# Performance work log

Measured on AMD Instinct MI355X. Metric: run time of the kernel, lower is better.

The kernel has to match this reference:

```python
import jax, jax.numpy as jnp
import numpy as np

B, S, H = 2, 2048, 2048
N_HEADS, N_KV = 16, 4
HEAD_DIM = H // N_HEADS  # 128
ROPE_THETA = 10000.0


def _rope_tables(seq_len, dim, theta):
    inv_freq = 1.0 / (theta ** (jnp.arange(0, dim, 2, dtype=jnp.float32) / dim))
    t = jnp.arange(seq_len, dtype=jnp.float32)
    freqs = jnp.outer(t, inv_freq)                 # [S, dim/2]
    emb = jnp.concatenate([freqs, freqs], axis=-1)  # [S, dim]
    return jnp.cos(emb), jnp.sin(emb)


def _rotate_half(x):
    x1, x2 = jnp.split(x, 2, axis=-1)
    return jnp.concatenate([-x2, x1], axis=-1)


def setup_inputs() -> dict:
    key = jax.random.key(0)
    ks = jax.random.split(key, 8)
    sc = 0.02
    return {
        "hidden_states": jax.random.normal(ks[0], (B, S, H), jnp.float32),
        "Wq": jax.random.normal(ks[1], (H, N_HEADS * HEAD_DIM), jnp.float32) * sc,
        "bq": jax.random.normal(ks[2], (N_HEADS * HEAD_DIM,), jnp.float32) * sc,
        "Wk": jax.random.normal(ks[3], (H, N_KV * HEAD_DIM), jnp.float32) * sc,
        "bk": jax.random.normal(ks[4], (N_KV * HEAD_DIM,), jnp.float32) * sc,
        "Wv": jax.random.normal(ks[5], (H, N_KV * HEAD_DIM), jnp.float32) * sc,
        "bv": jax.random.normal(ks[6], (N_KV * HEAD_DIM,), jnp.float32) * sc,
        "Wo": jax.random.normal(ks[7], (N_HEADS * HEAD_DIM, H), jnp.float32) * sc,
    }


def reference(hidden_states, Wq, bq, Wk, bk, Wv, bv, Wo):
    bsz, q_len, _ = hidden_states.shape
    q = hidden_states @ Wq + bq  # [B,S,nH*D]
    k = hidden_states @ Wk + bk  # [B,S,nKV*D]
    v = hidden_states @ Wv + bv
    q = q.reshape(bsz, q_len, N_HEADS, HEAD_DIM).transpose(0, 2, 1, 3)   # [B,nH,S,D]
    k = k.reshape(bsz, q_len, N_KV, HEAD_DIM).transpose(0, 2, 1, 3)      # [B,nKV,S,D]
    v = v.reshape(bsz, q_len, N_KV, HEAD_DIM).transpose(0, 2, 1, 3)

    cos, sin = _rope_tables(q_len, HEAD_DIM, ROPE_THETA)  # [S,D]
    cos = cos[None, None].astype(q.dtype)  # [1,1,S,D]
    sin = sin[None, None].astype(q.dtype)
    q = q * cos + _rotate_half(q) * sin
    k = k * cos + _rotate_half(k) * sin

    groups = N_HEADS // N_KV
    k_rep = jnp.repeat(k, groups, axis=1)  # [B,nH,S,D]
    v_rep = jnp.repeat(v, groups, axis=1)

    scale = 1.0 / np.sqrt(HEAD_DIM)
    scores = jnp.einsum("bhqd,bhkd->bhqk", q, k_rep) * scale
    attn = jax.nn.softmax(scores.astype(jnp.float32), axis=-1).astype(q.dtype)
    out = jnp.einsum("bhqk,bhkd->bhqd", attn, v_rep)
    out = out.transpose(0, 2, 1, 3).reshape(bsz, q_len, N_HEADS * HEAD_DIM)
    return out @ Wo
```

## Files before the change

kernel.cpp:

```cpp
#include <hip/hip_runtime.h>
#include <stdint.h>
#include <math.h>

typedef unsigned int u32;
typedef __bf16 bf16x8 __attribute__((ext_vector_type(8)));
typedef float  f32x4  __attribute__((ext_vector_type(4)));
typedef float  f32x16 __attribute__((ext_vector_type(16)));
typedef unsigned int u32x4 __attribute__((ext_vector_type(4)));
typedef unsigned short u16x4 __attribute__((ext_vector_type(4)));
typedef unsigned short u16x8 __attribute__((ext_vector_type(8)));

#define DEV __device__ __forceinline__

DEV unsigned short f2b(float f) {
  u32 x = __builtin_bit_cast(u32, f);
  u32 r = (x + 0x7fffu + ((x >> 16) & 1u)) >> 16;
  return (unsigned short)r;
}
DEV float b2f(unsigned short u) { return __builtin_bit_cast(float, ((u32)u) << 16); }

DEV u32 cvtpk_bf16(float lo, float hi) {
  u32 r;
  asm("v_cvt_pk_bf16_f32 %0, %1, %2" : "=v"(r) : "v"(lo), "v"(hi));
  return r;
}
DEV void pl32swap(u32& a, u32& b) {
  asm("v_permlane32_swap_b32 %0, %1" : "+v"(a), "+v"(b));
}

DEV void gl2lds16(const void* g, void* l) {
  __builtin_amdgcn_global_load_lds((const __attribute__((address_space(1))) u32*)g,
                                   (__attribute__((address_space(3))) u32*)l, 16, 0, 0);
}

__global__ __launch_bounds__(256) void prep_k(
    const float* __restrict__ X, const float* __restrict__ Wq,
    const float* __restrict__ Wk, const float* __restrict__ Wv,
    const float* __restrict__ Wo, float* __restrict__ ct, float* __restrict__ st,
    unsigned short* __restrict__ Xp, unsigned short* __restrict__ Wcat,
    unsigned short* __restrict__ Wop) {
  __shared__ float t[32][33];
  const int tid = threadIdx.x;
  int bx = blockIdx.x;
  if (bx < 512) {
    int i = (bx << 8) + tid;
    int d = i & 63;
    float inv = powf(10000.0f, -(float)d / 64.0f);
    float a = (float)(i >> 6) * inv;
    ct[i] = cosf(a);
    st[i] = sinf(a);
    return;
  }
  bx -= 512;
  if (bx < 4096) {
    int i = (bx << 8) + tid;
    int k8 = i & 255, m = i >> 8;
    const float4* p = (const float4*)(X + (size_t)m * 2048 + (k8 << 3));
    float4 v0 = p[0], v1 = p[1];
    u16x8 r = { f2b(v0.x), f2b(v0.y), f2b(v0.z), f2b(v0.w),
                f2b(v1.x), f2b(v1.y), f2b(v1.z), f2b(v1.w) };
    int kt = k8 >> 2, ko = (k8 & 3) << 3;
    *(u16x8*)(Xp + ((size_t)kt * 4096 + m) * 32 + ko) = r;
    return;
  }
  bx -= 4096;
  int wx = bx % 160, wy = bx / 160;
  const float* src; unsigned short* dst; int Nd, Ncat, ncOff, nb;
  if (wx < 64)       { src = Wq; dst = Wcat; Nd = 2048; Ncat = 3072; ncOff = 0;    nb = wx; }
  else if (wx < 80)  { src = Wk; dst = Wcat; Nd = 512;  Ncat = 3072; ncOff = 2048; nb = wx - 64; }
  else if (wx < 96)  { src = Wv; dst = Wcat; Nd = 512;  Ncat = 3072; ncOff = 2560; nb = wx - 80; }
  else               { src = Wo; dst = Wop;  Nd = 2048; Ncat = 2048; ncOff = 0;    nb = wx - 96; }
  int n0 = nb << 5, k0 = wy << 5;
  int tx = tid & 31, ty = tid >> 5;
  for (int i2 = ty; i2 < 32; i2 += 8) t[i2][tx] = src[(size_t)(k0 + i2) * Nd + n0 + tx];
  __syncthreads();
  for (int i2 = ty; i2 < 32; i2 += 8)
    dst[((size_t)(k0 >> 5) * Ncat + ncOff + n0 + i2) * 32 + tx] = f2b(t[tx][i2]);
}

template <int MODE, int GX, int SLOTS>
__global__ __launch_bounds__(256, SLOTS == 2 ? 4 : 3) void gemm3s_k(
    const unsigned short* __restrict__ Ap, const unsigned short* __restrict__ Bp,
    float* __restrict__ outF, unsigned short* __restrict__ outQ,
    unsigned short* __restrict__ outK, unsigned short* __restrict__ outV,
    const float* __restrict__ bq_, const float* __restrict__ bk_,
    const float* __restrict__ bv_, const float* __restrict__ ctab,
    const float* __restrict__ stab, int Mtot, int Ntot) {
  constexpr int NST = 64;
  constexpr int RING = SLOTS * 16384;
  constexpr int SHMB = (RING > 33280) ? RING : 33280;
  __shared__ alignas(16) char shm[SHMB];
  unsigned short* Al = (unsigned short*)shm;
  unsigned short* Bl = (unsigned short*)(shm + SLOTS * 8192);
  float* ex = (float*)shm;

  const int tid = threadIdx.x, lane = tid & 63, wid = tid >> 6;
  const int wm = wid >> 1, wn = wid & 1;
  const int cl = lane & 15, g = lane >> 4;

  const int bid = blockIdx.x;
  const int by = ((bid & 7) << 2) + ((bid >> 3) / GX);
  const int bx = (bid >> 3) % GX;
  const int row0 = by << 7, col0 = bx << 7;

  const int c0 = wid, c1 = wid + 4;
  const int sr0 = (c0 << 4) + (lane >> 2);
  const int sr1 = (c1 << 4) + (lane >> 2);
  const int sl0 = (lane & 3) ^ ((sr0 >> 1) & 3);
  const int sl1 = (lane & 3) ^ ((sr1 >> 1) & 3);
  const size_t dA = (size_t)Mtot * 32, dB = (size_t)Ntot * 32;
  const unsigned short* pa0 = Ap + (size_t)(row0 + sr0) * 32 + (sl0 << 3);
  const unsigned short* pa1 = Ap + (size_t)(row0 + sr1) * 32 + (sl1 << 3);
  const unsigned short* pb0 = Bp + (size_t)(col0 + sr0) * 32 + (sl0 << 3);
  const unsigned short* pb1 = Bp + (size_t)(col0 + sr1) * 32 + (sl1 << 3);
  const int ld0 = (c0 << 9) + (lane << 3);
  const int ld1 = (c1 << 9) + (lane << 3);

  int sslot = 0;
  auto stage = [&]() {
    const int bb = sslot << 12;
    gl2lds16(pa0, &Al[bb + ld0]);
    gl2lds16(pa1, &Al[bb + ld1]);
    gl2lds16(pb0, &Bl[bb + ld0]);
    gl2lds16(pb1, &Bl[bb + ld1]);
    pa0 += dA; pa1 += dA; pb0 += dB; pb1 += dB;
    sslot = sslot == SLOTS - 1 ? 0 : sslot + 1;
  };

  int aoff[4], boff[4];
#pragma unroll
  for (int m = 0; m < 4; ++m) {
    int row = (wm << 6) + (m << 4) + cl;
    aoff[m] = (row << 5) + ((g ^ ((row >> 1) & 3)) << 3);
    row = (wn << 6) + (m << 4) + cl;
    boff[m] = (row << 5) + ((g ^ ((row >> 1) & 3)) << 3);
  }

  f32x4 acc[4][4];
#pragma unroll
  for (int m = 0; m < 4; ++m)
#pragma unroll
    for (int n = 0; n < 4; ++n) acc[m][n] = (f32x4){0.f, 0.f, 0.f, 0.f};

#define STEP(RS, DO_STAGE)                                                         \
  do {                                                                             \
    const int bb_ = (RS) << 12;                                                    \
    bf16x8 af[4], bfr[4];                                                          \
    _Pragma("unroll") for (int m = 0; m < 4; ++m)                                  \
        af[m] = *(const bf16x8*)&Al[bb_ + aoff[m]];                                \
    _Pragma("unroll") for (int n = 0; n < 4; ++n)                                  \
        bfr[n] = *(const bf16x8*)&Bl[bb_ + boff[n]];                               \
    if (DO_STAGE) stage();                                                         \
    __builtin_amdgcn_s_setprio(1);                                                 \
    _Pragma("unroll") for (int m = 0; m < 4; ++m)                                  \
      _Pragma("unroll") for (int n = 0; n < 4; ++n)                                \
        acc[m][n] = __builtin_amdgcn_mfma_f32_16x16x32_bf16(af[m], bfr[n],         \
                                                            acc[m][n], 0, 0, 0);  \
    __builtin_amdgcn_s_setprio(0);                                                 \
  } while (0)

#pragma unroll
  for (int i = 0; i < SLOTS - 1; ++i) stage();
  if constexpr (SLOTS == 3) { asm volatile("s_waitcnt vmcnt(4)" ::: "memory"); }
  else                      { asm volatile("s_waitcnt vmcnt(0)" ::: "memory"); }
  __builtin_amdgcn_s_barrier();

  int rslot = 0;
  for (int s = 0; s < NST - (SLOTS - 1); ++s) {
    STEP(rslot, true);
    if constexpr (SLOTS == 3) { asm volatile("s_waitcnt vmcnt(4)" ::: "memory"); }
    else                      { asm volatile("s_waitcnt vmcnt(0)" ::: "memory"); }
    __builtin_amdgcn_s_barrier();
    rslot = rslot == SLOTS - 1 ? 0 : rslot + 1;
  }
  if constexpr (SLOTS == 3) {
    STEP(rslot, false);
    asm volatile("s_waitcnt vmcnt(0)" ::: "memory");
    __builtin_amdgcn_s_barrier();
    rslot = rslot == SLOTS - 1 ? 0 : rslot + 1;
  }
  STEP(rslot, false);
#undef STEP
  __syncthreads();

  if constexpr (MODE == 0) {
#pragma unroll
    for (int mt = 0; mt < 4; ++mt) {
      int rbase = row0 + (wm << 6) + (mt << 4) + (g << 2);
#pragma unroll
      for (int nt = 0; nt < 4; ++nt) {
        int col = col0 + (wn << 6) + (nt << 4) + cl;
#pragma unroll
        for (int r = 0; r < 4; ++r)
          outF[(size_t)(rbase + r) * Ntot + col] = acc[mt][nt][r];
      }
    }
  } else {
    if (col0 >= 2560) {
#pragma unroll
      for (int mt = 0; mt < 4; ++mt) {
        int rbase = row0 + (wm << 6) + (mt << 4) + (g << 2);
#pragma unroll
        for (int nt = 0; nt < 4; ++nt) {
          int col = col0 + (wn << 6) + (nt << 4) + cl;
          int c2 = col - 2560, kk = c2 >> 7, d = c2 & 127;
          float bv2 = bv_[c2];
#pragma unroll
          for (int r = 0; r < 4; ++r) {
            int rr = rbase + r;
            int bb = rr >> 11, ss = rr & 2047;
            outV[((((size_t)bb << 2) + kk) * 128 + d) * 2048 + ss] =
                f2b(acc[mt][nt][r] + bv2);
          }
        }
      }
    } else {
      const bool isQ = col0 < 2048;
      const float* bias = isQ ? (bq_ + col0) : (bk_ + (col0 - 2048));
      if (wn == 1) {
#pragma unroll
        for (int mt = 0; mt < 4; ++mt) {
#pragma unroll
          for (int nt = 0; nt < 4; ++nt) {
            int d2 = (nt << 4) + cl;
            float b2 = bias[64 + d2];
#pragma unroll
            for (int r = 0; r < 4; ++r) {
              int lrow = (wm << 6) + (mt << 4) + (g << 2) + r;
              ex[lrow * 65 + d2] = acc[mt][nt][r] + b2;
            }
          }
        }
      }
      __syncthreads();
      if (wn == 0) {
        const int hh = isQ ? (col0 >> 7) : ((col0 - 2048) >> 7);
#pragma unroll
        for (int mt = 0; mt < 4; ++mt) {
#pragma unroll
          for (int nt = 0; nt < 4; ++nt) {
            int d = (nt << 4) + cl;
            float b1 = bias[d];
#pragma unroll
            for (int r = 0; r < 4; ++r) {
              int lrow = (wm << 6) + (mt << 4) + (g << 2) + r;
              int grow = row0 + lrow;
              int bb = grow >> 11, ss = grow & 2047;
              float x1 = acc[mt][nt][r] + b1;
              float x2 = ex[lrow * 65 + d];
              float c = ctab[ss * 64 + d], sn = stab[ss * 64 + d];
              float o1 = x1 * c - x2 * sn;
              float o2 = x2 * c + x1 * sn;
              if (isQ) {
                o1 *= (0.08838834764831845f * 1.4426950408889634f);
                o2 *= (0.08838834764831845f * 1.4426950408889634f);
              }
              unsigned short* dp = isQ
                  ? outQ + ((((size_t)bb << 4) + hh) * 2048 + ss) * 128
                  : outK + ((((size_t)bb << 2) + hh) * 2048 + ss) * 128;
              dp[d] = f2b(o1);
              dp[d + 64] = f2b(o2);
            }
          }
        }
      }
    }
  }
}

__global__ __launch_bounds__(256, 2) void attn2_k(
    const unsigned short* __restrict__ Qb, const unsigned short* __restrict__ Kb,
    const unsigned short* __restrict__ Vt, unsigned short* __restrict__ AOp) {
  __shared__ alignas(16) unsigned short Ks[2][64 * 128];
  __shared__ alignas(16) unsigned short Vs[2][64 * 128];

  const int tid = threadIdx.x, lane = tid & 63, wid = tid >> 6;
  const int hw = blockIdx.x;
  const int work = ((hw & 7) << 6) | (hw >> 3);
  const int qblk = work & 15, bh = work >> 4;
  const int b = bh >> 4, h = bh & 15, kvh = h >> 2;
  const int q0 = qblk << 7;
  const int cl = lane & 31, hi = lane >> 5;

  const unsigned short* Qp = Qb + ((size_t)(b * 16 + h) << 11) * 128;
  const unsigned short* Kp = Kb + ((size_t)(b * 4 + kvh) << 11) * 128;
  const unsigned short* Vp = Vt + ((size_t)(b * 4 + kvh) << 7) * 2048;

  const int qrow = q0 + (wid << 5) + cl;
  bf16x8 qf[8];
#pragma unroll
  for (int c = 0; c < 8; ++c)
    qf[c] = *(const bf16x8*)(Qp + (size_t)qrow * 128 + (c << 4) + (hi << 3));

  const unsigned short* ksrc[4];
  int kldo[4];
  const unsigned short* vsrc[4];
  int vldo[4];
#pragma unroll
  for (int i = 0; i < 4; ++i) {
    {
      int row = (wid << 4) + (i << 2) + (lane >> 4);
      int sl = (lane & 15) ^ (row & 15);
      ksrc[i] = Kp + ((size_t)row << 7) + (sl << 3);
      kldo[i] = (wid << 11) + (i << 9) + (lane << 3);
    }
    {
      int c = (wid << 2) + i;
      int r = (c << 2) + (lane >> 4);
      int sp = lane & 15;
      int slog = sp ^ (r & 15);
      int d = (slog & 8) ? (r + 64) : r;
      int kvo = (slog & 7) << 3;
      vsrc[i] = Vp + (size_t)d * 2048 + kvo;
      vldo[i] = (c << 9) + (lane << 3);
    }
  }

  auto stage = [&](int t, int buf) {
#pragma unroll
    for (int i = 0; i < 4; ++i)
      gl2lds16(ksrc[i] + ((size_t)t << 13), &Ks[buf][kldo[i]]);
#pragma unroll
    for (int i = 0; i < 4; ++i)
      gl2lds16(vsrc[i] + (t << 6), &Vs[buf][vldo[i]]);
  };

  f32x16 o[4];
#pragma unroll
  for (int dt = 0; dt < 4; ++dt)
#pragma unroll
    for (int r = 0; r < 16; ++r) o[dt][r] = 0.f;
  float l = 0.f;

  auto pack8 = [&](float a0, float a1, float a2, float a3,
                   float a4, float a5, float a6, float a7) -> u32x4 {
    u32 x0 = cvtpk_bf16(a0, a1);
    u32 y0 = cvtpk_bf16(a4, a5);
    u32 x1 = cvtpk_bf16(a2, a3);
    u32 y1 = cvtpk_bf16(a6, a7);
    pl32swap(x0, y0);
    pl32swap(x1, y1);
    return (u32x4){x0, x1, y0, y1};
  };

  stage(0, 0);
  __syncthreads();

  for (int t = 0; t < 32; ++t) {
    const int buf = t & 1;
    if (t + 1 < 32) stage(t + 1, buf ^ 1);

    f32x16 s0, s1;
#pragma unroll
    for (int r = 0; r < 16; ++r) { s0[r] = 0.f; s1[r] = 0.f; }
    __builtin_amdgcn_s_setprio(1);
#pragma unroll
    for (int c = 0; c < 8; ++c) {
      int sl0 = ((c << 1) + hi) ^ (cl & 15);
      bf16x8 kf0 = *(const bf16x8*)&Ks[buf][(cl << 7) + (sl0 << 3)];
      s0 = __builtin_amdgcn_mfma_f32_32x32x16_bf16(kf0, qf[c], s0, 0, 0, 0);
    }
#pragma unroll
    for (int c = 0; c < 8; ++c) {
      int row = 32 + cl;
      int sl1 = ((c << 1) + hi) ^ (row & 15);
      bf16x8 kf1 = *(const bf16x8*)&Ks[buf][(row << 7) + (sl1 << 3)];
      s1 = __builtin_amdgcn_mfma_f32_32x32x16_bf16(kf1, qf[c], s1, 0, 0, 0);
    }
    __builtin_amdgcn_s_setprio(0);

    float sum = 0.f;
#pragma unroll
    for (int r = 0; r < 16; ++r) { s0[r] = __builtin_amdgcn_exp2f(s0[r]); sum += s0[r]; }
#pragma unroll
    for (int r = 0; r < 16; ++r) { s1[r] = __builtin_amdgcn_exp2f(s1[r]); sum += s1[r]; }
    l += sum;

    u32x4 w0 = pack8(s0[0], s0[1], s0[2], s0[3], s0[4], s0[5], s0[6], s0[7]);
    u32x4 w1 = pack8(s0[8], s0[9], s0[10], s0[11], s0[12], s0[13], s0[14], s0[15]);
    u32x4 w2 = pack8(s1[0], s1[1], s1[2], s1[3], s1[4], s1[5], s1[6], s1[7]);
    u32x4 w3 = pack8(s1[8], s1[9], s1[10], s1[11], s1[12], s1[13], s1[14], s1[15]);
    bf16x8 pa0 = __builtin_bit_cast(bf16x8, w0);
    bf16x8 pa1 = __builtin_bit_cast(bf16x8, w1);
    bf16x8 pa2 = __builtin_bit_cast(bf16x8, w2);
    bf16x8 pa3 = __builtin_bit_cast(bf16x8, w3);

    __builtin_amdgcn_s_setprio(1);
#pragma unroll
    for (int dt = 0; dt < 4; ++dt) {
      int d = (dt << 5) + cl;
      int row = d & 63;
      int rx = row & 15;
      int sb = row << 7;
      int bs = (dt & 2) << 2;
      bf16x8 vf0 = *(const bf16x8*)&Vs[buf][sb + (((bs + 0 + hi) ^ rx) << 3)];
      o[dt] = __builtin_amdgcn_mfma_f32_32x32x16_bf16(vf0, pa0, o[dt], 0, 0, 0);
      bf16x8 vf1 = *(const bf16x8*)&Vs[buf][sb + (((bs + 2 + hi) ^ rx) << 3)];
      o[dt] = __builtin_amdgcn_mfma_f32_32x32x16_bf16(vf1, pa1, o[dt], 0, 0, 0);
      bf16x8 vf2 = *(const bf16x8*)&Vs[buf][sb + (((bs + 4 + hi) ^ rx) << 3)];
      o[dt] = __builtin_amdgcn_mfma_f32_32x32x16_bf16(vf2, pa2, o[dt], 0, 0, 0);
      bf16x8 vf3 = *(const bf16x8*)&Vs[buf][sb + (((bs + 6 + hi) ^ rx) << 3)];
      o[dt] = __builtin_amdgcn_mfma_f32_32x32x16_bf16(vf3, pa3, o[dt], 0, 0, 0);
    }
    __builtin_amdgcn_s_setprio(0);
    __syncthreads();
  }

  float inv = 1.0f / (l + __shfl_xor(l, 32));
  const int rowi = b * 2048 + qrow;
#pragma unroll
  for (int dt = 0; dt < 4; ++dt) {
    unsigned short* base = AOp + (((size_t)((h << 2) + dt)) * 4096 + rowi) * 32;
#pragma unroll
    for (int rq = 0; rq < 4; ++rq) {
      u16x4 pk = { f2b(o[dt][(rq << 2) + 0] * inv), f2b(o[dt][(rq << 2) + 1] * inv),
                   f2b(o[dt][(rq << 2) + 2] * inv), f2b(o[dt][(rq << 2) + 3] * inv) };
      *(u16x4*)(base + (rq << 3) + (hi << 2)) = pk;
    }
  }
}

extern "C" void kernel_launch(void* const* d_in, const int* in_sizes, int n_in,
                              void* d_out, int out_size, void* d_ws, size_t ws_size,
                              hipStream_t stream) {
  const float* X  = (const float*)d_in[0];
  const float* Wq = (const float*)d_in[1];
  const float* bq = (const float*)d_in[2];
  const float* Wk = (const float*)d_in[3];
  const float* bk = (const float*)d_in[4];
  const float* Wv = (const float*)d_in[5];
  const float* bv = (const float*)d_in[6];
  const float* Wo = (const float*)d_in[7];
  float* out = (float*)d_out;

  char* ws = (char*)d_ws;
  size_t off = 0;
  auto alloc = [&](size_t bytes) {
    char* p = ws + off;
    off += (bytes + 255) & ~(size_t)255;
    return p;
  };
  unsigned short* Xp   = (unsigned short*)alloc(4096ull * 2048 * 2);
  unsigned short* Wcat = (unsigned short*)alloc(3072ull * 2048 * 2);
  unsigned short* Wop  = (unsigned short*)alloc(2048ull * 2048 * 2);
  unsigned short* Qb   = (unsigned short*)alloc(2ull * 16 * 2048 * 128 * 2);
  unsigned short* Kb   = (unsigned short*)alloc(2ull * 4 * 2048 * 128 * 2);
  unsigned short* Vt   = (unsigned short*)alloc(2ull * 4 * 128 * 2048 * 2);
  unsigned short* AOp  = (unsigned short*)alloc(4096ull * 2048 * 2);
  float* ctab = (float*)alloc(2048ull * 64 * 4);
  float* stab = (float*)alloc(2048ull * 64 * 4);

  prep_k<<<dim3(14848), dim3(256), 0, stream>>>(X, Wq, Wk, Wv, Wo,
                                                ctab, stab, Xp, Wcat, Wop);

  gemm3s_k<3, 24, 2><<<dim3(768), dim3(256), 0, stream>>>(
      Xp, Wcat, nullptr, Qb, Kb, Vt, bq, bk, bv, ctab, stab, 4096, 3072);

  attn2_k<<<dim3(512), dim3(256), 0, stream>>>(Qb, Kb, Vt, AOp);

  gemm3s_k<0, 16, 2><<<dim3(512), dim3(256), 0, stream>>>(
      AOp, Wop, out, nullptr, nullptr, nullptr, nullptr, nullptr, nullptr,
      nullptr, nullptr, 4096, 2048);
}
```

Measured before the change: 187.5 us.

## Split attention KV range in two with a separate merge kernel

Attention now runs as 1024 blocks, each covering half of the key/value sequence with 32-row K/V tiles, and the launch bounds are raised to allow four blocks per CU. Each block writes an unnormalized bf16 partial output and its row sums. A new merge kernel adds the two partials and divides by the combined sums. The aim is more parallelism and smaller LDS tiles per block. In exchange it adds an extra kernel launch, roughly 48 MB of extra global traffic, and extra bf16 rounding on the unnormalized partial outputs.

Result: slower. 233.5 us (+24.6%).

```diff
diff --git a/kernel.cpp b/kernel.cpp
--- a/kernel.cpp
+++ b/kernel.cpp
@@ -268,23 +268,25 @@
   }
 }
 
-__global__ __launch_bounds__(256, 2) void attn2_k(
+__global__ __launch_bounds__(256, 4) void attn3_k(
     const unsigned short* __restrict__ Qb, const unsigned short* __restrict__ Kb,
-    const unsigned short* __restrict__ Vt, unsigned short* __restrict__ AOp) {
-  __shared__ alignas(16) unsigned short Ks[2][64 * 128];
-  __shared__ alignas(16) unsigned short Vs[2][64 * 128];
+    const unsigned short* __restrict__ Vt, unsigned short* __restrict__ AO0,
+    unsigned short* __restrict__ AO1, float* __restrict__ lpart) {
+  __shared__ alignas(16) unsigned short Ks[2][32 * 128];
+  __shared__ alignas(16) unsigned short Vs[2][32 * 128];
 
   const int tid = threadIdx.x, lane = tid & 63, wid = tid >> 6;
   const int hw = blockIdx.x;
-  const int work = ((hw & 7) << 6) | (hw >> 3);
-  const int qblk = work & 15, bh = work >> 4;
+  const int work = ((hw & 7) << 7) | (hw >> 3);
+  const int qblk = work & 15, split = (work >> 4) & 1, bh = work >> 5;
   const int b = bh >> 4, h = bh & 15, kvh = h >> 2;
   const int q0 = qblk << 7;
+  const int kvbase = split << 10;
   const int cl = lane & 31, hi = lane >> 5;
 
-  const unsigned short* Qp = Qb + ((size_t)(b * 16 + h) << 11) * 128;
-  const unsigned short* Kp = Kb + ((size_t)(b * 4 + kvh) << 11) * 128;
-  const unsigned short* Vp = Vt + ((size_t)(b * 4 + kvh) << 7) * 2048;
+  const unsigned short* Qp = Qb + ((size_t)bh << 11) * 128;
+  const unsigned short* Kp = Kb + ((size_t)(b * 4 + kvh) << 11) * 128 + ((size_t)kvbase << 7);
+  const unsigned short* Vp = Vt + ((size_t)(b * 4 + kvh) << 7) * 2048 + kvbase;
 
   const int qrow = q0 + (wid << 5) + cl;
   bf16x8 qf[8];
@@ -292,37 +294,29 @@
   for (int c = 0; c < 8; ++c)
     qf[c] = *(const bf16x8*)(Qp + (size_t)qrow * 128 + (c << 4) + (hi << 3));
 
-  const unsigned short* ksrc[4];
-  int kldo[4];
-  const unsigned short* vsrc[4];
-  int vldo[4];
-#pragma unroll
-  for (int i = 0; i < 4; ++i) {
-    {
-      int row = (wid << 4) + (i << 2) + (lane >> 4);
-      int sl = (lane & 15) ^ (row & 15);
-      ksrc[i] = Kp + ((size_t)row << 7) + (sl << 3);
-      kldo[i] = (wid << 11) + (i << 9) + (lane << 3);
-    }
-    {
-      int c = (wid << 2) + i;
-      int r = (c << 2) + (lane >> 4);
-      int sp = lane & 15;
-      int slog = sp ^ (r & 15);
-      int d = (slog & 8) ? (r + 64) : r;
-      int kvo = (slog & 7) << 3;
-      vsrc[i] = Vp + (size_t)d * 2048 + kvo;
-      vldo[i] = (c << 9) + (lane << 3);
-    }
+  const unsigned short* ksrc[2];
+  const unsigned short* vsrc[2];
+  int ldo[2];
+#pragma unroll
+  for (int i = 0; i < 2; ++i) {
+    int c = (wid << 1) + i;
+    int r = (c << 2) + (lane >> 4);
+    ldo[i] = (c << 9) + (lane << 3);
+    int ksl = (lane & 15) ^ (r & 15);
+    ksrc[i] = Kp + ((size_t)r << 7) + (ksl << 3);
+    int slog = (lane & 15) ^ (r & 15);
+    int vd = ((slog >> 2) << 5) + r;
+    int vkv = (slog & 3) << 3;
+    vsrc[i] = Vp + (size_t)vd * 2048 + vkv;
   }
 
   auto stage = [&](int t, int buf) {
 #pragma unroll
-    for (int i = 0; i < 4; ++i)
-      gl2lds16(ksrc[i] + ((size_t)t << 13), &Ks[buf][kldo[i]]);
-#pragma unroll
-    for (int i = 0; i < 4; ++i)
-      gl2lds16(vsrc[i] + (t << 6), &Vs[buf][vldo[i]]);
+    for (int i = 0; i < 2; ++i)
+      gl2lds16(ksrc[i] + ((size_t)t << 12), &Ks[buf][ldo[i]]);
+#pragma unroll
+    for (int i = 0; i < 2; ++i)
+      gl2lds16(vsrc[i] + (t << 5), &Vs[buf][ldo[i]]);
   };
 
   f32x16 o[4];
@@ -350,9 +344,9 @@
     const int buf = t & 1;
     if (t + 1 < 32) stage(t + 1, buf ^ 1);
 
-    f32x16 s0, s1;
-#pragma unroll
-    for (int r = 0; r < 16; ++r) { s0[r] = 0.f; s1[r] = 0.f; }
+    f32x16 s0;
+#pragma unroll
+    for (int r = 0; r < 16; ++r) s0[r] = 0.f;
     __builtin_amdgcn_s_setprio(1);
 #pragma unroll
     for (int c = 0; c < 8; ++c) {
@@ -360,64 +354,66 @@
       bf16x8 kf0 = *(const bf16x8*)&Ks[buf][(cl << 7) + (sl0 << 3)];
       s0 = __builtin_amdgcn_mfma_f32_32x32x16_bf16(kf0, qf[c], s0, 0, 0, 0);
     }
-#pragma unroll
-    for (int c = 0; c < 8; ++c) {
-      int row = 32 + cl;
-      int sl1 = ((c << 1) + hi) ^ (row & 15);
-      bf16x8 kf1 = *(const bf16x8*)&Ks[buf][(row << 7) + (sl1 << 3)];
-      s1 = __builtin_amdgcn_mfma_f32_32x32x16_bf16(kf1, qf[c], s1, 0, 0, 0);
-    }
     __builtin_amdgcn_s_setprio(0);
 
     float sum = 0.f;
 #pragma unroll
     for (int r = 0; r < 16; ++r) { s0[r] = __builtin_amdgcn_exp2f(s0[r]); sum += s0[r]; }
-#pragma unroll
-    for (int r = 0; r < 16; ++r) { s1[r] = __builtin_amdgcn_exp2f(s1[r]); sum += s1[r]; }
     l += sum;
 
     u32x4 w0 = pack8(s0[0], s0[1], s0[2], s0[3], s0[4], s0[5], s0[6], s0[7]);
     u32x4 w1 = pack8(s0[8], s0[9], s0[10], s0[11], s0[12], s0[13], s0[14], s0[15]);
-    u32x4 w2 = pack8(s1[0], s1[1], s1[2], s1[3], s1[4], s1[5], s1[6], s1[7]);
-    u32x4 w3 = pack8(s1[8], s1[9], s1[10], s1[11], s1[12], s1[13], s1[14], s1[15]);
     bf16x8 pa0 = __builtin_bit_cast(bf16x8, w0);
     bf16x8 pa1 = __builtin_bit_cast(bf16x8, w1);
-    bf16x8 pa2 = __builtin_bit_cast(bf16x8, w2);
-    bf16x8 pa3 = __builtin_bit_cast(bf16x8, w3);
 
     __builtin_amdgcn_s_setprio(1);
 #pragma unroll
     for (int dt = 0; dt < 4; ++dt) {
-      int d = (dt << 5) + cl;
-      int row = d & 63;
-      int rx = row & 15;
-      int sb = row << 7;
-      int bs = (dt & 2) << 2;
-      bf16x8 vf0 = *(const bf16x8*)&Vs[buf][sb + (((bs + 0 + hi) ^ rx) << 3)];
+      int rx = cl & 15;
+      int sb = cl << 7;
+      bf16x8 vf0 = *(const bf16x8*)&Vs[buf][sb + ((((dt << 2) + 0 + hi) ^ rx) << 3)];
       o[dt] = __builtin_amdgcn_mfma_f32_32x32x16_bf16(vf0, pa0, o[dt], 0, 0, 0);
-      bf16x8 vf1 = *(const bf16x8*)&Vs[buf][sb + (((bs + 2 + hi) ^ rx) << 3)];
+      bf16x8 vf1 = *(const bf16x8*)&Vs[buf][sb + ((((dt << 2) + 2 + hi) ^ rx) << 3)];
       o[dt] = __builtin_amdgcn_mfma_f32_32x32x16_bf16(vf1, pa1, o[dt], 0, 0, 0);
-      bf16x8 vf2 = *(const bf16x8*)&Vs[buf][sb + (((bs + 4 + hi) ^ rx) << 3)];
-      o[dt] = __builtin_amdgcn_mfma_f32_32x32x16_bf16(vf2, pa2, o[dt], 0, 0, 0);
-      bf16x8 vf3 = *(const bf16x8*)&Vs[buf][sb + (((bs + 6 + hi) ^ rx) << 3)];
-      o[dt] = __builtin_amdgcn_mfma_f32_32x32x16_bf16(vf3, pa3, o[dt], 0, 0, 0);
     }
     __builtin_amdgcn_s_setprio(0);
     __syncthreads();
   }
 
-  float inv = 1.0f / (l + __shfl_xor(l, 32));
+  unsigned short* AOdst = split ? AO1 : AO0;
   const int rowi = b * 2048 + qrow;
 #pragma unroll
   for (int dt = 0; dt < 4; ++dt) {
-    unsigned short* base = AOp + (((size_t)((h << 2) + dt)) * 4096 + rowi) * 32;
+    unsigned short* base = AOdst + (((size_t)((h << 2) + dt)) * 4096 + rowi) * 32;
 #pragma unroll
     for (int rq = 0; rq < 4; ++rq) {
-      u16x4 pk = { f2b(o[dt][(rq << 2) + 0] * inv), f2b(o[dt][(rq << 2) + 1] * inv),
-                   f2b(o[dt][(rq << 2) + 2] * inv), f2b(o[dt][(rq << 2) + 3] * inv) };
+      u16x4 pk = { f2b(o[dt][(rq << 2) + 0]), f2b(o[dt][(rq << 2) + 1]),
+                   f2b(o[dt][(rq << 2) + 2]), f2b(o[dt][(rq << 2) + 3]) };
       *(u16x4*)(base + (rq << 3) + (hi << 2)) = pk;
     }
   }
+  float lt = l + __shfl_xor(l, 32);
+  if (hi == 0) lpart[(split << 16) + (bh << 11) + qrow] = lt;
+}
+
+__global__ __launch_bounds__(256) void merge_k(
+    unsigned short* __restrict__ AO0, const unsigned short* __restrict__ AO1,
+    const float* __restrict__ lpart) {
+  int idx = blockIdx.x * 256 + threadIdx.x;
+  size_t flat = (size_t)idx << 3;
+  int panel = (int)(flat >> 17);
+  int rem = (int)(flat & 131071);
+  int rowi = rem >> 5;
+  int h = panel >> 2;
+  int b = rowi >> 11, q = rowi & 2047;
+  int li = (((b << 4) + h) << 11) + q;
+  float inv = 1.0f / (lpart[li] + lpart[65536 + li]);
+  u16x8 a = *(const u16x8*)(AO0 + flat);
+  u16x8 c = *(const u16x8*)(AO1 + flat);
+  u16x8 r;
+#pragma unroll
+  for (int e = 0; e < 8; ++e) r[e] = f2b((b2f(a[e]) + b2f(c[e])) * inv);
+  *(u16x8*)(AO0 + flat) = r;
 }
 
 extern "C" void kernel_launch(void* const* d_in, const int* in_sizes, int n_in,
@@ -446,7 +442,9 @@
   unsigned short* Qb   = (unsigned short*)alloc(2ull * 16 * 2048 * 128 * 2);
   unsigned short* Kb   = (unsigned short*)alloc(2ull * 4 * 2048 * 128 * 2);
   unsigned short* Vt   = (unsigned short*)alloc(2ull * 4 * 128 * 2048 * 2);
-  unsigned short* AOp  = (unsigned short*)alloc(4096ull * 2048 * 2);
+  unsigned short* AO0  = (unsigned short*)alloc(4096ull * 2048 * 2);
+  unsigned short* AO1  = (unsigned short*)alloc(4096ull * 2048 * 2);
+  float* lpart = (float*)alloc(2ull * 65536 * 4);
   float* ctab = (float*)alloc(2048ull * 64 * 4);
   float* stab = (float*)alloc(2048ull * 64 * 4);
 
@@ -456,9 +454,10 @@
   gemm3s_k<3, 24, 2><<<dim3(768), dim3(256), 0, stream>>>(
       Xp, Wcat, nullptr, Qb, Kb, Vt, bq, bk, bv, ctab, stab, 4096, 3072);
 
-  attn2_k<<<dim3(512), dim3(256), 0, stream>>>(Qb, Kb, Vt, AOp);
+  attn3_k<<<dim3(1024), dim3(256), 0, stream>>>(Qb, Kb, Vt, AO0, AO1, lpart);
+  merge_k<<<dim3(4096), dim3(256), 0, stream>>>(AO0, AO1, lpart);
 
   gemm3s_k<0, 16, 2><<<dim3(512), dim3(256), 0, stream>>>(
-      AOp, Wop, out, nullptr, nullptr, nullptr, nullptr, nullptr, nullptr,
+      AO0, Wop, out, nullptr, nullptr, nullptr, nullptr, nullptr, nullptr,
       nullptr, nullptr, 4096, 2048);
 }
```
